# Optimization experiments

Hardware: AMD Instinct MI355X
Metric: run time of the kernel (lower is better)

Reference implementation:

```python
import jax, jax.numpy as jnp
import numpy as np

N = 100000      # nodes
E = 1600000     # edges
IN_DIM = 256
H = 128         # hidden_mlp == hidden_gnn
Z = 32          # latent_dim
HD = 128        # hidden_dec


def _lin(k, fan_in, fan_out):
    # torch nn.Linear default init: U(-1/sqrt(fan_in), 1/sqrt(fan_in))
    kw, kb = jax.random.split(k)
    lim = 1.0 / np.sqrt(fan_in)
    W = jax.random.uniform(kw, (fan_in, fan_out), jnp.float32, -lim, lim)
    b = jax.random.uniform(kb, (fan_out,), jnp.float32, -lim, lim)
    return W, b


def setup_inputs() -> dict:
    key = jax.random.key(0)
    ks = jax.random.split(key, 16)
    x = jax.random.normal(ks[0], (N, IN_DIM), jnp.float32)
    edge_index = jax.random.randint(ks[1], (2, E), 0, N, jnp.int64)
    edge_attr = jax.random.uniform(ks[2], (E,), jnp.float32)

    W1, b1 = _lin(ks[3], IN_DIM, H)       # encoder mlp layer 1
    W2, b2 = _lin(ks[4], H, H)            # encoder mlp layer 2
    Wrel1, brel1 = _lin(ks[5], H, H)      # gnn1 lin_rel
    Wroot1, _ = _lin(ks[6], H, H)         # gnn1 lin_root (no bias)
    Wrel2, brel2 = _lin(ks[7], H, H)      # gnn2 lin_rel
    Wroot2, _ = _lin(ks[8], H, H)         # gnn2 lin_root
    Wmu, bmu = _lin(ks[9], H, Z)
    Wlv, blv = _lin(ks[10], H, Z)
    Wd1, bd1 = _lin(ks[11], Z, HD)
    Wd2, bd2 = _lin(ks[12], HD, IN_DIM)
    eps = jax.random.normal(ks[13], (N, Z), jnp.float32)  # reparam noise (fixed)

    return dict(x=x, edge_index=edge_index, edge_attr=edge_attr,
                W1=W1, b1=b1, W2=W2, b2=b2,
                Wrel1=Wrel1, brel1=brel1, Wroot1=Wroot1,
                Wrel2=Wrel2, brel2=brel2, Wroot2=Wroot2,
                Wmu=Wmu, bmu=bmu, Wlv=Wlv, blv=blv,
                Wd1=Wd1, bd1=bd1, Wd2=Wd2, bd2=bd2, eps=eps)


def _graph_conv(h, src, dst, w, Wrel, brel, Wroot):
    # PyG GraphConv (aggr='add'): out_i = lin_rel(sum_{j->i} w_ji * h_j) + lin_root(h_i)
    msgs = h[src] * w[:, None]                       # [E, H] gather
    agg = jax.ops.segment_sum(msgs, dst, num_segments=N)  # [N, H] scatter-add
    return agg @ Wrel + brel + h @ Wroot


def reference(x, edge_index, edge_attr,
              W1, b1, W2, b2,
              Wrel1, brel1, Wroot1,
              Wrel2, brel2, Wroot2,
              Wmu, bmu, Wlv, blv,
              Wd1, bd1, Wd2, bd2, eps):
    src, dst = edge_index[0], edge_index[1]
    # encoder MLP
    h = jax.nn.relu(x @ W1 + b1)
    h = jax.nn.relu(h @ W2 + b2)
    # two GraphConv message-passing layers with ReLU
    h = jax.nn.relu(_graph_conv(h, src, dst, edge_attr, Wrel1, brel1, Wroot1))
    h = jax.nn.relu(_graph_conv(h, src, dst, edge_attr, Wrel2, brel2, Wroot2))
    # heads
    mu = h @ Wmu + bmu
    logvar = h @ Wlv + blv
    # reparameterize with fixed eps
    z = mu + eps * jnp.exp(0.5 * logvar)
    # decoder MLP
    x_recon = jax.nn.relu(z @ Wd1 + bd1) @ Wd2 + bd2
    return x_recon, mu, logvar, z
```

## Files before the change

kernel.cpp:

```cpp
#include <hip/hip_runtime.h>
#include <math.h>

#define NN 100000
#define EE 1600000
#define NB 1563

typedef _Float16 f16;
typedef __attribute__((ext_vector_type(2))) _Float16 f16x2;
typedef __attribute__((ext_vector_type(8))) _Float16 f16x8;
typedef __attribute__((ext_vector_type(4))) float f32x4;
typedef unsigned int u32;

__device__ __forceinline__ float frelu(float v){ return v > 0.f ? v : 0.f; }

__device__ __forceinline__ f32x4 mfma16(f16x8 a, f16x8 b, f32x4 c){
    return __builtin_amdgcn_mfma_f32_16x16x32_f16(a, b, c, 0, 0, 0);
}

__device__ __forceinline__ int2 nt_load_int2(const int2* p){
    long long v = __builtin_nontemporal_load((const long long*)p);
    int2 r; r.x = (int)(v & 0xFFFFFFFFll); r.y = (int)(v >> 32);
    return r;
}

__global__ __launch_bounds__(256) void hist_pack(const int* __restrict__ dst,
                                                 int* __restrict__ blockhist,
                                                 const float* __restrict__ W1,
                                                 const float* __restrict__ W2,
                                                 const float* __restrict__ Wrel1,
                                                 const float* __restrict__ Wroot1,
                                                 const float* __restrict__ Wrel2,
                                                 const float* __restrict__ Wroot2,
                                                 const float* __restrict__ Wd1,
                                                 const float* __restrict__ Wd2,
                                                 const float* __restrict__ Wmu,
                                                 const float* __restrict__ Wlv,
                                                 f16* __restrict__ pack)
{
    __shared__ int cntS[NB];
    const int t = threadIdx.x;
    if (blockIdx.x < 250) {
        const int blk = blockIdx.x;
        for (int i = t; i < NB; i += 256) cntS[i] = 0;
        __syncthreads();
        const int ebase = blk * 6400;
        #pragma unroll
        for (int i = 0; i < 25; i++) {
            int k = dst[ebase + i * 256 + t] >> 6;
            atomicAdd(&cntS[k], 1);
        }
        __syncthreads();
        for (int i = t; i < NB; i += 256)
            blockhist[blk * NB + i] = cntS[i];
        return;
    }
    int tt = (blockIdx.x - 250) * 256 + t;
    float v;
    if (tt < 32768) {
        int l = tt;
        int j = l & 7, lane = (l >> 3) & 63, ct = (l >> 9) & 7, kk = l >> 12;
        int k = kk * 32 + ((lane >> 4) << 3) + j, c = (ct << 4) + (lane & 15);
        v = W1[k * 128 + c];
    } else if (tt < 49152) {
        int l = tt - 32768;
        int j = l & 7, lane = (l >> 3) & 63, ct = (l >> 9) & 7, kk = l >> 12;
        int k = kk * 32 + ((lane >> 4) << 3) + j, c = (ct << 4) + (lane & 15);
        v = W2[k * 128 + c];
    } else if (tt < 81920) {
        int l = tt - 49152;
        int j = l & 7, lane = (l >> 3) & 63, ct = (l >> 9) & 7, kk = l >> 12;
        int k = kk * 32 + ((lane >> 4) << 3) + j, c = (ct << 4) + (lane & 15);
        v = (k < 128) ? Wrel1[k * 128 + c] : Wroot1[(k - 128) * 128 + c];
    } else if (tt < 114688) {
        int l = tt - 81920;
        int j = l & 7, lane = (l >> 3) & 63, ct = (l >> 9) & 7, kk = l >> 12;
        int k = kk * 32 + ((lane >> 4) << 3) + j, c = (ct << 4) + (lane & 15);
        v = (k < 128) ? Wrel2[k * 128 + c] : Wroot2[(k - 128) * 128 + c];
    } else if (tt < 118784) {
        int l = tt - 114688;
        int j = l & 7, lane = (l >> 3) & 63, ct = (l >> 9) & 7;
        int k = ((lane >> 4) << 3) + j, c = (ct << 4) + (lane & 15);
        v = Wd1[k * 128 + c];
    } else if (tt < 151552) {
        int l = tt - 118784;
        int j = l & 7, lane = (l >> 3) & 63, ct = (l >> 9) & 15, kk = l >> 13;
        int k = kk * 32 + ((lane >> 4) << 3) + j, c = (ct << 4) + (lane & 15);
        v = Wd2[k * 256 + c];
    } else {
        int l = tt - 151552;
        int j = l & 7, lane = (l >> 3) & 63, ct = (l >> 9) & 3, kk = l >> 11;
        int k = kk * 32 + ((lane >> 4) << 3) + j, c = (ct << 4) + (lane & 15);
        v = (c < 32) ? Wmu[k * 32 + c] : Wlv[k * 32 + (c - 32)];
    }
    pack[tt] = (f16)v;
}

template<int C>
__device__ __forceinline__ void stage_tile(const float* __restrict__ src, int nbase,
                                           f16* lds, int ldr, int colofs)
{
    const int t = threadIdx.x;
    #pragma unroll
    for (int i = 0; i < (64 * C / 4) / 256; i++) {
        int elem = t + i * 256;
        int row = elem / (C / 4);
        int c4  = elem % (C / 4);
        int srow = nbase + row; if (srow >= NN) srow = NN - 1;
        float4 v = *(const float4*)(src + (size_t)srow * C + c4 * 4);
        union { f16 h[4]; uint2 u; } cv;
        cv.h[0] = (f16)v.x; cv.h[1] = (f16)v.y; cv.h[2] = (f16)v.z; cv.h[3] = (f16)v.w;
        *(uint2*)&lds[row * ldr + colofs + c4 * 4] = cv.u;
    }
}

template<int C>
__device__ __forceinline__ void stage_tile_f16(const f16* __restrict__ src, int nbase,
                                               f16* lds, int ldr, int colofs)
{
    const int t = threadIdx.x;
    #pragma unroll
    for (int i = 0; i < (64 * C / 4) / 256; i++) {
        int elem = t + i * 256;
        int row = elem / (C / 4);
        int c4  = elem % (C / 4);
        int srow = nbase + row; if (srow >= NN) srow = NN - 1;
        uint2 v = *(const uint2*)(src + (size_t)srow * C + c4 * 4);
        *(uint2*)&lds[row * ldr + colofs + c4 * 4] = v;
    }
}

template<int K, int CT>
__device__ __forceinline__ void wave_gemm(const f16* lds, int ldr,
                                          const f16x8* __restrict__ wp, f32x4 acc[CT])
{
    const int lane = threadIdx.x & 63;
    const int wrow = (threadIdx.x >> 6) * 16;
    const int arow = wrow + (lane & 15);
    const int kofs = (lane >> 4) << 3;
    #pragma unroll
    for (int kk = 0; kk < K / 32; kk++) {
        f16x8 a = *(const f16x8*)&lds[arow * ldr + kk * 32 + kofs];
        #pragma unroll
        for (int ct = 0; ct < CT; ct++) {
            f16x8 b = wp[(kk * CT + ct) * 64 + lane];
            acc[ct] = mfma16(a, b, acc[ct]);
        }
    }
}

template<int CT>
__device__ __forceinline__ void zacc(f32x4 acc[CT])
{
    #pragma unroll
    for (int ct = 0; ct < CT; ct++) acc[ct] = f32x4{0.f, 0.f, 0.f, 0.f};
}

template<int CT, bool RELU>
__device__ __forceinline__ void store_f32(float* __restrict__ dst, int OUTC, int nbase,
                                          const float* __restrict__ bias, f32x4 acc[CT])
{
    const int lane = threadIdx.x & 63;
    const int wrow = (threadIdx.x >> 6) * 16;
    #pragma unroll
    for (int ct = 0; ct < CT; ct++) {
        int c = ct * 16 + (lane & 15);
        float bv = bias[c];
        #pragma unroll
        for (int r = 0; r < 4; r++) {
            int node = nbase + wrow + ((lane >> 4) << 2) + r;
            if (node < NN) {
                float v = acc[ct][r] + bv;
                if (RELU) v = frelu(v);
                dst[(size_t)node * OUTC + c] = v;
            }
        }
    }
}

template<int CT, bool RELU>
__device__ __forceinline__ void store_f16g(f16* __restrict__ dst, int OUTC, int nbase,
                                           const float* __restrict__ bias, f32x4 acc[CT])
{
    const int lane = threadIdx.x & 63;
    const int wrow = (threadIdx.x >> 6) * 16;
    #pragma unroll
    for (int ct = 0; ct < CT; ct++) {
        int c = ct * 16 + (lane & 15);
        float bv = bias[c];
        #pragma unroll
        for (int r = 0; r < 4; r++) {
            int node = nbase + wrow + ((lane >> 4) << 2) + r;
            if (node < NN) {
                float v = acc[ct][r] + bv;
                if (RELU) v = frelu(v);
                dst[(size_t)node * OUTC + c] = (f16)v;
            }
        }
    }
}

template<int CT>
__device__ __forceinline__ void store_lds_f16(f16* lds, int ldr,
                                              const float* __restrict__ bias, f32x4 acc[CT])
{
    const int lane = threadIdx.x & 63;
    const int wrow = (threadIdx.x >> 6) * 16;
    #pragma unroll
    for (int ct = 0; ct < CT; ct++) {
        int c = ct * 16 + (lane & 15);
        float bv = bias[c];
        #pragma unroll
        for (int r = 0; r < 4; r++) {
            int row = wrow + ((lane >> 4) << 2) + r;
            lds[row * ldr + c] = (f16)frelu(acc[ct][r] + bv);
        }
    }
}

__global__ __launch_bounds__(256) void colscan_enc(int* __restrict__ blockhist,
                                                   int* __restrict__ totals,
                                                   const float* __restrict__ x,
                                                   const f16x8* __restrict__ wp1,
                                                   const f16x8* __restrict__ wp2,
                                                   const float* __restrict__ b1,
                                                   const float* __restrict__ b2,
                                                   f16* __restrict__ out)
{
    __shared__ __align__(16) f16 shbuf[64 * 264 + 64 * 136];
    const int t = threadIdx.x;
    if (blockIdx.x < NB) {
        int* lds = (int*)shbuf;
        const int k = blockIdx.x;
        int v = (t < 250) ? blockhist[t * NB + k] : 0;
        lds[t] = v;
        __syncthreads();
        for (int off = 1; off < 256; off <<= 1) {
            int y = (t >= off) ? lds[t - off] : 0;
            __syncthreads();
            lds[t] += y;
            __syncthreads();
        }
        if (t < 250) blockhist[t * NB + k] = lds[t] - v;
        if (t == 255) totals[k] = lds[255];
        return;
    }
    f16* xs = shbuf;
    f16* h1 = shbuf + 64 * 264;
    const int nbase = (blockIdx.x - NB) * 64;
    stage_tile<256>(x, nbase, xs, 264, 0);
    __syncthreads();
    f32x4 acc[8];
    zacc<8>(acc);
    wave_gemm<256, 8>(xs, 264, wp1, acc);
    store_lds_f16<8>(h1, 136, b1, acc);
    __syncthreads();
    zacc<8>(acc);
    wave_gemm<128, 8>(h1, 136, wp2, acc);
    store_f16g<8, true>(out, 128, nbase, b2, acc);
}

__global__ __launch_bounds__(256) void scatter(const int* __restrict__ src,
                                               const int* __restrict__ dst,
                                               const float* __restrict__ ea,
                                               const int* __restrict__ totals,
                                               const int* __restrict__ blockhist,
                                               int* __restrict__ bs_g,
                                               int2* __restrict__ tmp)
{
    __shared__ int bsS[NB + 1];
    __shared__ int tmpS[256];
    __shared__ int carryS;
    __shared__ int prefS[NB];
    __shared__ int cntS[NB];
    const int t = threadIdx.x, blk = blockIdx.x;
    if (t == 0) carryS = 0;
    __syncthreads();
    for (int c = 0; c < 7; c++) {
        int idx = c * 256 + t;
        int val = (idx < NB) ? totals[idx] : 0;
        tmpS[t] = val;
        __syncthreads();
        for (int off = 1; off < 256; off <<= 1) {
            int y = (t >= off) ? tmpS[t - off] : 0;
            __syncthreads();
            tmpS[t] += y;
            __syncthreads();
        }
        if (idx < NB) bsS[idx] = carryS + tmpS[t] - val;
        __syncthreads();
        if (t == 255) carryS += tmpS[255];
        __syncthreads();
    }
    if (t == 0) bsS[NB] = carryS;
    for (int i = t; i < NB; i += 256) {
        prefS[i] = blockhist[blk * NB + i];
        cntS[i] = 0;
    }
    __syncthreads();
    if (blk == 0)
        for (int i = t; i < NB + 1; i += 256) bs_g[i] = bsS[i];
    const int ebase = blk * 6400;
    #pragma unroll
    for (int i = 0; i < 25; i++) {
        int e = ebase + i * 256 + t;
        int d = dst[e];
        int k = d >> 6;
        int rank = atomicAdd(&cntS[k], 1);
        int pos = bsS[k] + prefS[k] + rank;
        tmp[pos] = make_int2(src[e] | ((d & 63) << 17), __float_as_int(ea[e]));
    }
}

__global__ __launch_bounds__(256) void bucket_sort(const int2* __restrict__ tmp,
                                                   const int* __restrict__ bs_g,
                                                   int2* __restrict__ pairs,
                                                   int* __restrict__ offsets,
                                                   int* __restrict__ counts)
{
    __shared__ int hist[64], excl[64], cursor[64];
    const int t = threadIdx.x, k = blockIdx.x;
    const int start = bs_g[k], end = bs_g[k + 1];
    if (t < 64) hist[t] = 0;
    __syncthreads();
    for (int i = start + t; i < end; i += 256)
        atomicAdd(&hist[(tmp[i].x >> 17) & 63], 1);
    __syncthreads();
    if (t == 0) {
        int run = 0;
        #pragma unroll
        for (int j = 0; j < 64; j++) { excl[j] = run; cursor[j] = run; run += hist[j]; }
    }
    __syncthreads();
    for (int i = start + t; i < end; i += 256) {
        int2 e = tmp[i];
        int local = (e.x >> 17) & 63;
        int rank = atomicAdd(&cursor[local], 1);
        pairs[start + rank] = make_int2(e.x & 0x1FFFF, e.y);
    }
    if (t < 64) {
        int node = (k << 6) + t;
        if (node < NN) {
            counts[node]  = hist[t];
            offsets[node] = start + excl[t] + hist[t];
        }
    }
}

__global__ __launch_bounds__(256) void agg_q(const f16* __restrict__ h,
                                             const int2* __restrict__ pairs,
                                             const int* __restrict__ offsets,
                                             const int* __restrict__ counts,
                                             f16* __restrict__ out)
{
    const int gt   = blockIdx.x * 256 + threadIdx.x;
    const int node = gt >> 4;
    const int ch   = gt & 15;
    const int end  = offsets[node];
    int i = end - counts[node];
    float acc[8];
    #pragma unroll
    for (int j = 0; j < 8; j++) acc[j] = 0.f;
    const uint4* __restrict__ h16 = (const uint4*)h;
    for (; i + 4 <= end; i += 4) {
        int2 p0 = nt_load_int2(pairs + i);
        int2 p1 = nt_load_int2(pairs + i + 1);
        int2 p2 = nt_load_int2(pairs + i + 2);
        int2 p3 = nt_load_int2(pairs + i + 3);
        uint4 r0 = h16[(size_t)p0.x * 16 + ch];
        uint4 r1 = h16[(size_t)p1.x * 16 + ch];
        uint4 r2 = h16[(size_t)p2.x * 16 + ch];
        uint4 r3 = h16[(size_t)p3.x * 16 + ch];
        float w0 = __int_as_float(p0.y), w1 = __int_as_float(p1.y);
        float w2 = __int_as_float(p2.y), w3 = __int_as_float(p3.y);
        const f16* e0 = (const f16*)&r0;
        const f16* e1 = (const f16*)&r1;
        const f16* e2 = (const f16*)&r2;
        const f16* e3 = (const f16*)&r3;
        #pragma unroll
        for (int j = 0; j < 8; j++) acc[j] = fmaf(w0, (float)e0[j], acc[j]);
        #pragma unroll
        for (int j = 0; j < 8; j++) acc[j] = fmaf(w1, (float)e1[j], acc[j]);
        #pragma unroll
        for (int j = 0; j < 8; j++) acc[j] = fmaf(w2, (float)e2[j], acc[j]);
        #pragma unroll
        for (int j = 0; j < 8; j++) acc[j] = fmaf(w3, (float)e3[j], acc[j]);
    }
    for (; i < end; ++i) {
        int2 p0 = nt_load_int2(pairs + i);
        uint4 r0 = h16[(size_t)p0.x * 16 + ch];
        float w0 = __int_as_float(p0.y);
        const f16* e0 = (const f16*)&r0;
        #pragma unroll
        for (int j = 0; j < 8; j++) acc[j] = fmaf(w0, (float)e0[j], acc[j]);
    }
    union { f16 hh[8]; uint4 u; } cv;
    #pragma unroll
    for (int j = 0; j < 8; j++) cv.hh[j] = (f16)acc[j];
    ((uint4*)out)[(size_t)node * 16 + ch] = cv.u;
}

__global__ __launch_bounds__(256) void conv_mfma(const f16* __restrict__ agg,
                                                 const f16* __restrict__ h,
                                                 const f16x8* __restrict__ wp,
                                                 const float* __restrict__ brel,
                                                 f16* __restrict__ out)
{
    __shared__ __align__(16) f16 as_[64 * 264];
    const int nbase = blockIdx.x * 64;
    stage_tile_f16<128>(agg, nbase, as_, 264, 0);
    stage_tile_f16<128>(h,   nbase, as_, 264, 128);
    __syncthreads();
    f32x4 acc[8];
    zacc<8>(acc);
    wave_gemm<256, 8>(as_, 264, wp, acc);
    store_f16g<8, true>(out, 128, nbase, brel, acc);
}

__global__ __launch_bounds__(256) void tail2_mfma(const f16* __restrict__ h,
                                                  const f16x8* __restrict__ wp_hd,
                                                  const float* __restrict__ bmu,
                                                  const float* __restrict__ blv,
                                                  const f16x8* __restrict__ wp_d1,
                                                  const float* __restrict__ bd1,
                                                  const f16x8* __restrict__ wp_d2,
                                                  const float* __restrict__ bd2,
                                                  const float* __restrict__ eps,
                                                  float* __restrict__ out)
{
    __shared__ __align__(16) f16 hsA[64 * 136];
    __shared__ __align__(16) float muS[64 * 32];
    __shared__ __align__(16) float lvS[64 * 32];
    __shared__ __align__(16) f16 zf[64 * 40];
    const int nbase = blockIdx.x * 64;
    const int t = threadIdx.x;
    const int lane = t & 63;
    const int wrow = (t >> 6) * 16;

    stage_tile_f16<128>(h, nbase, hsA, 136, 0);
    __syncthreads();

    f32x4 acc4[4];
    zacc<4>(acc4);
    wave_gemm<128, 4>(hsA, 136, wp_hd, acc4);
    #pragma unroll
    for (int ct = 0; ct < 4; ct++) {
        int c = ct * 16 + (lane & 15);
        bool ismu = (c < 32);
        int cc = c & 31;
        float bv = ismu ? bmu[cc] : blv[cc];
        float* gbase = out + (ismu ? (size_t)25600000 : (size_t)28800000);
        float* sb = ismu ? muS : lvS;
        #pragma unroll
        for (int r = 0; r < 4; r++) {
            int row = wrow + ((lane >> 4) << 2) + r;
            int node = nbase + row;
            float v = acc4[ct][r] + bv;
            sb[row * 32 + cc] = v;
            if (node < NN) gbase[(size_t)node * 32 + cc] = v;
        }
    }
    __syncthreads();

    {
        const int node = t >> 2;
        const int ch0  = (t & 3) * 8;
        const int gn = nbase + node;
        const float* mu = &muS[node * 32 + ch0];
        const float* lv = &lvS[node * 32 + ch0];
        float4 e0 = make_float4(0.f, 0.f, 0.f, 0.f), e1 = e0;
        if (gn < NN) {
            const size_t g = (size_t)gn * 32 + ch0;
            e0 = *(const float4*)(eps + g);
            e1 = *(const float4*)(eps + g + 4);
        }
        float zv[8];
        zv[0] = fmaf(e0.x, expf(0.5f * lv[0]), mu[0]);
        zv[1] = fmaf(e0.y, expf(0.5f * lv[1]), mu[1]);
        zv[2] = fmaf(e0.z, expf(0.5f * lv[2]), mu[2]);
        zv[3] = fmaf(e0.w, expf(0.5f * lv[3]), mu[3]);
        zv[4] = fmaf(e1.x, expf(0.5f * lv[4]), mu[4]);
        zv[5] = fmaf(e1.y, expf(0.5f * lv[5]), mu[5]);
        zv[6] = fmaf(e1.z, expf(0.5f * lv[6]), mu[6]);
        zv[7] = fmaf(e1.w, expf(0.5f * lv[7]), mu[7]);
        if (gn < NN) {
            const size_t g = (size_t)gn * 32 + ch0;
            *(float4*)(out + 32000000 + g)     = make_float4(zv[0], zv[1], zv[2], zv[3]);
            *(float4*)(out + 32000000 + g + 4) = make_float4(zv[4], zv[5], zv[6], zv[7]);
        }
        #pragma unroll
        for (int j = 0; j < 8; j++) zf[node * 40 + ch0 + j] = (f16)zv[j];
    }
    __syncthreads();

    f32x4 acc8[8];
    zacc<8>(acc8);
    wave_gemm<32, 8>(zf, 40, wp_d1, acc8);
    store_lds_f16<8>(hsA, 136, bd1, acc8);
    __syncthreads();

    f32x4 acc16[16];
    zacc<16>(acc16);
    wave_gemm<128, 16>(hsA, 136, wp_d2, acc16);
    store_f32<16, false>(out, 256, nbase, bd2, acc16);
}

extern "C" void kernel_launch(void* const* d_in, const int* in_sizes, int n_in,
                              void* d_out, int out_size, void* d_ws, size_t ws_size,
                              hipStream_t stream)
{
    const float* x     = (const float*)d_in[0];
    const int*   ei    = (const int*)d_in[1];
    const float* ea    = (const float*)d_in[2];
    const float* W1    = (const float*)d_in[3];
    const float* b1    = (const float*)d_in[4];
    const float* W2    = (const float*)d_in[5];
    const float* b2    = (const float*)d_in[6];
    const float* Wrel1 = (const float*)d_in[7];
    const float* brel1 = (const float*)d_in[8];
    const float* Wroot1= (const float*)d_in[9];
    const float* Wrel2 = (const float*)d_in[10];
    const float* brel2 = (const float*)d_in[11];
    const float* Wroot2= (const float*)d_in[12];
    const float* Wmu   = (const float*)d_in[13];
    const float* bmu   = (const float*)d_in[14];
    const float* Wlv   = (const float*)d_in[15];
    const float* blv   = (const float*)d_in[16];
    const float* Wd1   = (const float*)d_in[17];
    const float* bd1   = (const float*)d_in[18];
    const float* Wd2   = (const float*)d_in[19];
    const float* bd2   = (const float*)d_in[20];
    const float* eps   = (const float*)d_in[21];
    float* out = (float*)d_out;

    char* ws = (char*)d_ws;
    int*  totals    = (int*) (ws);
    int*  blockhist = (int*) (ws + 8192);
    int*  bs_g      = (int*) (ws + 1571200);
    int2* tmp       = (int2*)(ws + 1577472);
    int2* pairs     = (int2*)(ws + 14377472);
    int*  offsets   = (int*) (ws + 27177472);
    int*  counts    = (int*) (ws + 27577472);
    f16*  pack      = (f16*) (ws + 27977472);
    f16*  B0        = (f16*) (ws + 28311552);
    f16*  B1        = (f16*) (ws + 53911552);

    const f16x8* wp_enc1  = (const f16x8*)(pack);
    const f16x8* wp_enc2  = (const f16x8*)(pack + 32768);
    const f16x8* wp_conv1 = (const f16x8*)(pack + 49152);
    const f16x8* wp_conv2 = (const f16x8*)(pack + 81920);
    const f16x8* wp_dec1  = (const f16x8*)(pack + 114688);
    const f16x8* wp_dec2  = (const f16x8*)(pack + 118784);
    const f16x8* wp_heads = (const f16x8*)(pack + 151552);

    const int* src = ei;
    const int* dst = ei + EE;

    hist_pack<<<874, 256, 0, stream>>>(dst, blockhist, W1, W2, Wrel1, Wroot1,
                                       Wrel2, Wroot2, Wd1, Wd2, Wmu, Wlv, pack);
    colscan_enc<<<NB + 1563, 256, 0, stream>>>(blockhist, totals, x,
                                               wp_enc1, wp_enc2, b1, b2, B0);
    scatter<<<250, 256, 0, stream>>>(src, dst, ea, totals, blockhist, bs_g, tmp);
    bucket_sort<<<NB, 256, 0, stream>>>(tmp, bs_g, pairs, offsets, counts);

    agg_q<<<6250, 256, 0, stream>>>(B0, pairs, offsets, counts, B1);
    conv_mfma<<<1563, 256, 0, stream>>>(B1, B0, wp_conv1, brel1, B1);
    agg_q<<<6250, 256, 0, stream>>>(B1, pairs, offsets, counts, B0);
    conv_mfma<<<1563, 256, 0, stream>>>(B0, B1, wp_conv2, brel2, B0);
    tail2_mfma<<<1563, 256, 0, stream>>>(B0, wp_heads, bmu, blv,
                                         wp_dec1, bd1, wp_dec2, bd2, eps, out);
}
```

Baseline: 397.2 us.

## Fuse edge aggregation into GraphConv MFMA kernel via shared-memory staging

Merges the gather/scatter aggregation kernel with the following dense conv GEMM kernel. Each block aggregates messages for its 64 nodes directly into shared memory alongside the root features, then runs the MFMA GEMM, which removes the global round-trip of the aggregated tensor and one launch per layer. In exchange, each thread now processes 4 nodes serially, so fewer threads are in flight to hide the latency of the random gathers.

New measurement: 405.9 us. 1.02x slower.

```diff
diff --git a/kernel.cpp b/kernel.cpp
--- a/kernel.cpp
+++ b/kernel.cpp
@@ -346,74 +346,71 @@
     }
 }
 
-__global__ __launch_bounds__(256) void agg_q(const f16* __restrict__ h,
-                                             const int2* __restrict__ pairs,
-                                             const int* __restrict__ offsets,
-                                             const int* __restrict__ counts,
-                                             f16* __restrict__ out)
-{
-    const int gt   = blockIdx.x * 256 + threadIdx.x;
-    const int node = gt >> 4;
-    const int ch   = gt & 15;
-    const int end  = offsets[node];
-    int i = end - counts[node];
-    float acc[8];
-    #pragma unroll
-    for (int j = 0; j < 8; j++) acc[j] = 0.f;
-    const uint4* __restrict__ h16 = (const uint4*)h;
-    for (; i + 4 <= end; i += 4) {
-        int2 p0 = nt_load_int2(pairs + i);
-        int2 p1 = nt_load_int2(pairs + i + 1);
-        int2 p2 = nt_load_int2(pairs + i + 2);
-        int2 p3 = nt_load_int2(pairs + i + 3);
-        uint4 r0 = h16[(size_t)p0.x * 16 + ch];
-        uint4 r1 = h16[(size_t)p1.x * 16 + ch];
-        uint4 r2 = h16[(size_t)p2.x * 16 + ch];
-        uint4 r3 = h16[(size_t)p3.x * 16 + ch];
-        float w0 = __int_as_float(p0.y), w1 = __int_as_float(p1.y);
-        float w2 = __int_as_float(p2.y), w3 = __int_as_float(p3.y);
-        const f16* e0 = (const f16*)&r0;
-        const f16* e1 = (const f16*)&r1;
-        const f16* e2 = (const f16*)&r2;
-        const f16* e3 = (const f16*)&r3;
-        #pragma unroll
-        for (int j = 0; j < 8; j++) acc[j] = fmaf(w0, (float)e0[j], acc[j]);
-        #pragma unroll
-        for (int j = 0; j < 8; j++) acc[j] = fmaf(w1, (float)e1[j], acc[j]);
-        #pragma unroll
-        for (int j = 0; j < 8; j++) acc[j] = fmaf(w2, (float)e2[j], acc[j]);
-        #pragma unroll
-        for (int j = 0; j < 8; j++) acc[j] = fmaf(w3, (float)e3[j], acc[j]);
-    }
-    for (; i < end; ++i) {
-        int2 p0 = nt_load_int2(pairs + i);
-        uint4 r0 = h16[(size_t)p0.x * 16 + ch];
-        float w0 = __int_as_float(p0.y);
-        const f16* e0 = (const f16*)&r0;
-        #pragma unroll
-        for (int j = 0; j < 8; j++) acc[j] = fmaf(w0, (float)e0[j], acc[j]);
-    }
-    union { f16 hh[8]; uint4 u; } cv;
-    #pragma unroll
-    for (int j = 0; j < 8; j++) cv.hh[j] = (f16)acc[j];
-    ((uint4*)out)[(size_t)node * 16 + ch] = cv.u;
-}
-
-__global__ __launch_bounds__(256) void conv_mfma(const f16* __restrict__ agg,
-                                                 const f16* __restrict__ h,
-                                                 const f16x8* __restrict__ wp,
-                                                 const float* __restrict__ brel,
-                                                 f16* __restrict__ out)
+__global__ __launch_bounds__(256) void agg_conv(const f16* __restrict__ h,
+                                                const int2* __restrict__ pairs,
+                                                const int* __restrict__ offsets,
+                                                const int* __restrict__ counts,
+                                                const f16x8* __restrict__ wp,
+                                                const float* __restrict__ brel,
+                                                f16* __restrict__ out)
 {
     __shared__ __align__(16) f16 as_[64 * 264];
     const int nbase = blockIdx.x * 64;
-    stage_tile_f16<128>(agg, nbase, as_, 264, 0);
-    stage_tile_f16<128>(h,   nbase, as_, 264, 128);
-    __syncthreads();
-    f32x4 acc[8];
-    zacc<8>(acc);
-    wave_gemm<256, 8>(as_, 264, wp, acc);
-    store_f16g<8, true>(out, 128, nbase, brel, acc);
+    const int t = threadIdx.x;
+    stage_tile_f16<128>(h, nbase, as_, 264, 128);
+    const int q = ((t >> 6) << 2) | ((t & 63) >> 4);
+    const int lane16 = t & 15;
+    const uint4* __restrict__ h16 = (const uint4*)h;
+    for (int n = 0; n < 4; n++) {
+        const int nl = q * 4 + n;
+        const int node = nbase + nl;
+        int end = 0, i = 0;
+        if (node < NN) { end = offsets[node]; i = end - counts[node]; }
+        float acc[8];
+        #pragma unroll
+        for (int j = 0; j < 8; j++) acc[j] = 0.f;
+        for (; i + 4 <= end; i += 4) {
+            int2 p0 = nt_load_int2(pairs + i);
+            int2 p1 = nt_load_int2(pairs + i + 1);
+            int2 p2 = nt_load_int2(pairs + i + 2);
+            int2 p3 = nt_load_int2(pairs + i + 3);
+            uint4 r0 = h16[(size_t)p0.x * 16 + lane16];
+            uint4 r1 = h16[(size_t)p1.x * 16 + lane16];
+            uint4 r2 = h16[(size_t)p2.x * 16 + lane16];
+            uint4 r3 = h16[(size_t)p3.x * 16 + lane16];
+            float w0 = __int_as_float(p0.y), w1 = __int_as_float(p1.y);
+            float w2 = __int_as_float(p2.y), w3 = __int_as_float(p3.y);
+            const f16* e0 = (const f16*)&r0;
+            const f16* e1 = (const f16*)&r1;
+            const f16* e2 = (const f16*)&r2;
+            const f16* e3 = (const f16*)&r3;
+            #pragma unroll
+            for (int j = 0; j < 8; j++) acc[j] = fmaf(w0, (float)e0[j], acc[j]);
+            #pragma unroll
+            for (int j = 0; j < 8; j++) acc[j] = fmaf(w1, (float)e1[j], acc[j]);
+            #pragma unroll
+            for (int j = 0; j < 8; j++) acc[j] = fmaf(w2, (float)e2[j], acc[j]);
+            #pragma unroll
+            for (int j = 0; j < 8; j++) acc[j] = fmaf(w3, (float)e3[j], acc[j]);
+        }
+        for (; i < end; ++i) {
+            int2 p0 = nt_load_int2(pairs + i);
+            uint4 r0 = h16[(size_t)p0.x * 16 + lane16];
+            float w0 = __int_as_float(p0.y);
+            const f16* e0 = (const f16*)&r0;
+            #pragma unroll
+            for (int j = 0; j < 8; j++) acc[j] = fmaf(w0, (float)e0[j], acc[j]);
+        }
+        union { f16 hh[8]; uint4 u; } cv;
+        #pragma unroll
+        for (int j = 0; j < 8; j++) cv.hh[j] = (f16)acc[j];
+        *(uint4*)&as_[nl * 264 + lane16 * 8] = cv.u;
+    }
+    __syncthreads();
+    f32x4 acc8[8];
+    zacc<8>(acc8);
+    wave_gemm<256, 8>(as_, 264, wp, acc8);
+    store_f16g<8, true>(out, 128, nbase, brel, acc8);
 }
 
 __global__ __launch_bounds__(256) void tail2_mfma(const f16* __restrict__ h,
@@ -562,10 +559,8 @@
     scatter<<<250, 256, 0, stream>>>(src, dst, ea, totals, blockhist, bs_g, tmp);
     bucket_sort<<<NB, 256, 0, stream>>>(tmp, bs_g, pairs, offsets, counts);
 
-    agg_q<<<6250, 256, 0, stream>>>(B0, pairs, offsets, counts, B1);
-    conv_mfma<<<1563, 256, 0, stream>>>(B1, B0, wp_conv1, brel1, B1);
-    agg_q<<<6250, 256, 0, stream>>>(B1, pairs, offsets, counts, B0);
-    conv_mfma<<<1563, 256, 0, stream>>>(B0, B1, wp_conv2, brel2, B0);
+    agg_conv<<<NB, 256, 0, stream>>>(B0, pairs, offsets, counts, wp_conv1, brel1, B1);
+    agg_conv<<<NB, 256, 0, stream>>>(B1, pairs, offsets, counts, wp_conv2, brel2, B0);
     tail2_mfma<<<1563, 256, 0, stream>>>(B0, wp_heads, bmu, blv,
                                          wp_dec1, bd1, wp_dec2, bd2, eps, out);
 }
```
